# Optimization experiments

Hardware: AMD Instinct MI355X
Metric: run time of the kernel (lower is better)

The kernel has to match this reference:

```python
import jax, jax.numpy as jnp
import numpy as np

T, H, W_, CIN, LAT, HID, OUT, NHL = 32, 64, 64, 3, 256, 256, 3, 3
OMEGA = 30.0  # SIREN sine frequency


def _uniform(key, shape, fan_in):
    b = np.sqrt(6.0 / fan_in) / OMEGA
    return jax.random.uniform(key, shape, jnp.float32, -b, b)


def setup_inputs() -> dict:
    key = jax.random.key(0)
    ks = jax.random.split(key, 10)
    return {
        "coords": jax.random.normal(ks[0], (T, H, W_, CIN), jnp.float32),
        "latents": jax.random.normal(ks[1], (T, LAT), jnp.float32),
        # shared SIREN weights (nf_net): W stored as (out, in) like nn.Linear
        "W0": _uniform(ks[2], (HID, CIN), CIN),
        "b0": jnp.zeros((HID,), jnp.float32),
        "Wh": _uniform(ks[3], (NHL, HID, HID), HID),
        "bh": jnp.zeros((NHL, HID), jnp.float32),
        "Wf": _uniform(ks[4], (OUT, HID), HID),
        "bf": jnp.zeros((OUT,), jnp.float32),
        # hypernet weight generators (hw_net), no bias
        "HW0": _uniform(ks[5], (HID * CIN, LAT), LAT),
        "HWh": _uniform(ks[6], (NHL, HID * HID, LAT), LAT),
        # hypernet bias generators (hb_net), no bias
        "HB": _uniform(ks[7], (NHL + 1, HID, LAT), LAT),
    }


def reference(coords, latents, W0, b0, Wh, bh, Wf, bf, HW0, HWh, HB):
    t = latents.shape[0]
    # per-frame hyper biases for all layers: (t, NHL+1, HID)
    hb = jnp.einsum('tl,khl->tkh', latents, HB)
    # layer 0: per-frame weight (t, HID, CIN)
    hw0 = (latents @ HW0.T).reshape(t, HID, CIN)
    x = coords  # (t,h,w,CIN)
    x = (x @ W0.T + b0
         + jnp.einsum('thwi,toi->thwo', x, hw0)
         + hb[:, 0][:, None, None, :])
    x = jnp.sin(OMEGA * x)
    for i in range(NHL):
        hw = (latents @ HWh[i].T).reshape(t, HID, HID)  # (t, HID, HID)
        x = (x @ Wh[i].T + bh[i]
             + jnp.einsum('thwi,toi->thwo', x, hw)
             + hb[:, i + 1][:, None, None, :])
        x = jnp.sin(OMEGA * x)
    return x @ Wf.T + bf  # (t,h,w,OUT)
```

## Files before the change

### kernel.cpp

```cpp
#include <hip/hip_runtime.h>
#include <cstdint>
#include <cstddef>

typedef __attribute__((ext_vector_type(8))) _Float16 f16x8;
typedef __attribute__((ext_vector_type(16))) float f32x16;

#define LO_SCALE 2048.0f
#define LO_INV   (1.0f / 2048.0f)

union H8 { f16x8 v; _Float16 h[8]; };

__global__ __launch_bounds__(256) void kc_small(
    const float* __restrict__ latents, const float* __restrict__ W0,
    const float* __restrict__ b0, const float* __restrict__ bh,
    const float* __restrict__ HW0, const float* __restrict__ HB,
    _Float16* __restrict__ w0blob, float* __restrict__ beff) {
  int id = blockIdx.x * 256 + threadIdx.x;
  if (id < 32768) {
    int t = id >> 10, rem = id & 1023;
    int r2 = rem & 127, part = r2 >> 6, lane = r2 & 63;
    int nf = rem >> 7;
    int o = nf * 32 + (lane & 31), kc = lane >> 5;
    const float* lat = latents + t * 256;
    H8 outv;
#pragma unroll
    for (int j = 0; j < 8; ++j) outv.h[j] = (_Float16)0.0f;
#pragma unroll
    for (int j = 0; j < 8; ++j) {
      int i = kc * 8 + j;
      if (i < 3) {
        const float* row = HW0 + (o * 3 + i) * 256;
        float s = W0[o * 3 + i];
        for (int k = 0; k < 256; k += 4)
          s += row[k] * lat[k] + row[k + 1] * lat[k + 1] +
               row[k + 2] * lat[k + 2] + row[k + 3] * lat[k + 3];
        _Float16 hi = (_Float16)s;
        outv.h[j] = part ? (_Float16)((s - (float)hi) * LO_SCALE) : hi;
      }
    }
    *(f16x8*)(w0blob + (size_t)id * 8) = outv.v;
  } else {
    int v = id - 32768;
    int t = v >> 10, k = (v >> 8) & 3, hm = v & 255;
    float base = (k == 0) ? b0[hm] : bh[(k - 1) * 256 + hm];
    const float* lat = latents + t * 256;
    const float* row = HB + (size_t)(k * 256 + hm) * 256;
    float s = base;
    for (int kk = 0; kk < 256; kk += 4)
      s += row[kk] * lat[kk] + row[kk + 1] * lat[kk + 1] +
           row[kk + 2] * lat[kk + 2] + row[kk + 3] * lat[kk + 3];
    beff[v] = s;
  }
}

__global__ __launch_bounds__(256) void ka_weff_blob(
    const float* __restrict__ latents, const float* __restrict__ Wh,
    const float* __restrict__ HWh, _Float16* __restrict__ whblob) {
  __shared__ float lat_t[8192];
  int tid = threadIdx.x, bid = blockIdx.x;
  int h = bid & 1, ks = (bid >> 1) & 15, nf = (bid >> 5) & 7, l = bid >> 8;

  {
    int f = tid >> 3, kb = (tid & 7) * 32;
#pragma unroll
    for (int m = 0; m < 32; m += 4) {
      float4 v = *(const float4*)(latents + f * 256 + kb + m);
      lat_t[(kb + m + 0) * 32 + f] = v.x;
      lat_t[(kb + m + 1) * 32 + f] = v.y;
      lat_t[(kb + m + 2) * 32 + f] = v.z;
      lat_t[(kb + m + 3) * 32 + f] = v.w;
    }
  }
  __syncthreads();

  int oo = tid >> 3, jj = tid & 7;
  int o = nf * 32 + oo;
  int i = ks * 16 + h * 8 + jj;
  int r = o * 256 + i;
  const float* rowp = HWh + ((size_t)l * 65536 + (size_t)r) * 256;

  float acc[32];
#pragma unroll
  for (int f = 0; f < 32; ++f) acc[f] = 0.f;

  float curf[16], nxtf[16];
#pragma unroll
  for (int q = 0; q < 4; ++q)
    *(float4*)(curf + q * 4) = *(const float4*)(rowp + q * 4);

  for (int kc = 0; kc < 16; ++kc) {
    if (kc < 15) {
#pragma unroll
      for (int q = 0; q < 4; ++q)
        *(float4*)(nxtf + q * 4) = *(const float4*)(rowp + (kc + 1) * 16 + q * 4);
    }
    const float* lp = lat_t + kc * 512;
#pragma unroll
    for (int m = 0; m < 16; ++m) {
      float hw = curf[m];
#pragma unroll
      for (int fq = 0; fq < 8; ++fq) {
        float4 lv = *(const float4*)(lp + m * 32 + fq * 4);
        acc[fq * 4 + 0] += hw * lv.x;
        acc[fq * 4 + 1] += hw * lv.y;
        acc[fq * 4 + 2] += hw * lv.z;
        acc[fq * 4 + 3] += hw * lv.w;
      }
    }
#pragma unroll
    for (int q = 0; q < 16; ++q) curf[q] = nxtf[q];
  }

  float whv = Wh[l * 65536 + r];
  size_t cbase = (size_t)(nf * 16 + ks) * 1024 + (size_t)h * 256 + (size_t)tid;
#pragma unroll
  for (int t = 0; t < 32; ++t) {
    float w = acc[t] + whv;
    _Float16 hi = (_Float16)w;
    _Float16 lo = (_Float16)((w - (float)hi) * LO_SCALE);
    size_t b = (size_t)(t * 3 + l) * 131072 + cbase;
    whblob[b] = hi;
    whblob[b + 512] = lo;
  }
}

__global__ __launch_bounds__(512, 4) void kb_siren(
    const float* __restrict__ coords, const _Float16* __restrict__ whblob,
    const _Float16* __restrict__ w0blob, const float* __restrict__ beff,
    const float* __restrict__ Wf, const float* __restrict__ bf,
    float* __restrict__ out) {
  __shared__ _Float16 xs_hi[64 * 264];
  __shared__ _Float16 xs_lo[64 * 264];
  __shared__ float wf_s[768];
  __shared__ float red[1536];
  int tid = threadIdx.x;
  int bid0 = blockIdx.x;
  int bid = (bid0 & 7) * 256 + (bid0 >> 3);
  int t = bid >> 6, tile = bid & 63;
  int wv = tid >> 6, lane = tid & 63, col = lane & 31, h = lane >> 5;

  if (tid < 192) *(float4*)(wf_s + tid * 4) = *(const float4*)(Wf + tid * 4);
  if (tid < 64) {
    const float* cp = coords + (size_t)(t * 4096 + tile * 64 + tid) * 3;
    float c0 = cp[0], c1 = cp[1], c2 = cp[2];
    H8 hv, lv, z;
#pragma unroll
    for (int j = 0; j < 8; ++j) { hv.h[j] = (_Float16)0.f; lv.h[j] = (_Float16)0.f; z.h[j] = (_Float16)0.f; }
    _Float16 h0 = (_Float16)c0, h1 = (_Float16)c1, h2 = (_Float16)c2;
    hv.h[0] = h0; hv.h[1] = h1; hv.h[2] = h2;
    lv.h[0] = (_Float16)((c0 - (float)h0) * LO_SCALE);
    lv.h[1] = (_Float16)((c1 - (float)h1) * LO_SCALE);
    lv.h[2] = (_Float16)((c2 - (float)h2) * LO_SCALE);
    *(f16x8*)(xs_hi + tid * 264) = hv.v;
    *(f16x8*)(xs_lo + tid * 264) = lv.v;
    *(f16x8*)(xs_hi + tid * 264 + 8) = z.v;
    *(f16x8*)(xs_lo + tid * 264 + 8) = z.v;
  }
  __syncthreads();

  f32x16 accA[2], accB[2];

  auto init_bias = [&](int bk) {
    const float* bp = beff + ((t * 4 + bk) << 8) + wv * 32 + h * 4;
#pragma unroll
    for (int rq = 0; rq < 4; ++rq) {
      float4 bvv = *(const float4*)(bp + rq * 8);
      float ba[4];
      *(float4*)ba = bvv;
#pragma unroll
      for (int q = 0; q < 4; ++q) {
        accA[0][rq * 4 + q] = ba[q];
        accA[1][rq * 4 + q] = ba[q];
        accB[0][rq * 4 + q] = 0.f;
        accB[1][rq * 4 + q] = 0.f;
      }
    }
  };

  auto load_a = [&](const _Float16* blobL, int NS, int ks, f16x8 (&a)[2]) {
    const _Float16* p = blobL + (size_t)((wv * NS + ks) * 2) * 512 + lane * 8;
    a[0] = *(const f16x8*)p;
    a[1] = *(const f16x8*)(p + 512);
  };

  auto load_b = [&](int ks, f16x8 (&b)[2][2]) {
#pragma unroll
    for (int pf = 0; pf < 2; ++pf) {
      int off = (pf * 32 + col) * 264 + ks * 16 + h * 8;
      b[pf][0] = *(const f16x8*)(xs_hi + off);
      b[pf][1] = *(const f16x8*)(xs_lo + off);
    }
  };

  auto mfma6 = [&](f16x8 (&a)[2], f16x8 (&b)[2][2]) {
    accA[0] = __builtin_amdgcn_mfma_f32_32x32x16_f16(a[0], b[0][0], accA[0], 0, 0, 0);
    accA[1] = __builtin_amdgcn_mfma_f32_32x32x16_f16(a[0], b[1][0], accA[1], 0, 0, 0);
    accB[0] = __builtin_amdgcn_mfma_f32_32x32x16_f16(a[0], b[0][1], accB[0], 0, 0, 0);
    accB[1] = __builtin_amdgcn_mfma_f32_32x32x16_f16(a[0], b[1][1], accB[1], 0, 0, 0);
    accB[0] = __builtin_amdgcn_mfma_f32_32x32x16_f16(a[1], b[0][0], accB[0], 0, 0, 0);
    accB[1] = __builtin_amdgcn_mfma_f32_32x32x16_f16(a[1], b[1][0], accB[1], 0, 0, 0);
  };

  auto epilogue = [&]() {
#pragma unroll
    for (int pf = 0; pf < 2; ++pf)
#pragma unroll
      for (int r = 0; r < 16; ++r)
        accA[pf][r] = __sinf(30.0f * (accA[pf][r] + accB[pf][r] * LO_INV));
    __syncthreads();
#pragma unroll
    for (int pf = 0; pf < 2; ++pf)
#pragma unroll
      for (int g = 0; g < 2; ++g) {
        float seq[8];
#pragma unroll
        for (int q = 0; q < 4; ++q) {
          float oa = accA[pf][8 * g + q];
          float ob = accA[pf][8 * g + 4 + q];
          float send = h ? oa : ob;
          float recv = __shfl_xor(send, 32, 64);
          seq[q]     = h ? recv : oa;
          seq[4 + q] = h ? ob : recv;
        }
        H8 hv, lv;
#pragma unroll
        for (int j = 0; j < 8; ++j) {
          _Float16 hi = (_Float16)seq[j];
          hv.h[j] = hi;
          lv.h[j] = (_Float16)((seq[j] - (float)hi) * LO_SCALE);
        }
        int off = (pf * 32 + col) * 264 + wv * 32 + g * 16 + h * 8;
        *(f16x8*)(xs_hi + off) = hv.v;
        *(f16x8*)(xs_lo + off) = lv.v;
      }
    __syncthreads();
  };

  init_bias(0);
  {
    f16x8 a[2], b[2][2];
    load_a(w0blob + (size_t)t * 8192, 1, 0, a);
    load_b(0, b);
    mfma6(a, b);
  }
  epilogue();

  for (int li = 0; li < 3; ++li) {
    init_bias(li + 1);
    const _Float16* bl = whblob + (size_t)(t * 3 + li) * 131072;
#pragma unroll
    for (int ks = 0; ks < 16; ++ks) {
      f16x8 a[2], b[2][2];
      load_a(bl, 16, ks, a);
      load_b(ks, b);
      mfma6(a, b);
    }
    epilogue();
  }

  {
    float pc0 = 0.f, pc1 = 0.f, pc2 = 0.f;
    int px = tid & 63, kq = tid >> 6;
#pragma unroll
    for (int cc = 0; cc < 4; ++cc) {
      int k0 = kq * 32 + cc * 8;
      H8 hv, lv;
      hv.v = *(const f16x8*)(xs_hi + px * 264 + k0);
      lv.v = *(const f16x8*)(xs_lo + px * 264 + k0);
#pragma unroll
      for (int j = 0; j < 8; ++j) {
        float xv = (float)hv.h[j] + (float)lv.h[j] * LO_INV;
        pc0 += xv * wf_s[k0 + j];
        pc1 += xv * wf_s[256 + k0 + j];
        pc2 += xv * wf_s[512 + k0 + j];
      }
    }
    red[(kq * 64 + px) * 3 + 0] = pc0;
    red[(kq * 64 + px) * 3 + 1] = pc1;
    red[(kq * 64 + px) * 3 + 2] = pc2;
    __syncthreads();
    if (tid < 192) {
      int p2 = tid / 3, c = tid - p2 * 3;
      float s = bf[c];
#pragma unroll
      for (int q = 0; q < 8; ++q) s += red[(q * 64 + p2) * 3 + c];
      out[(size_t)(t * 4096 + tile * 64 + p2) * 3 + c] = s;
    }
  }
}

extern "C" void kernel_launch(void* const* d_in, const int* in_sizes, int n_in,
                              void* d_out, int out_size, void* d_ws, size_t ws_size,
                              hipStream_t stream) {
  const float* coords  = (const float*)d_in[0];
  const float* latents = (const float*)d_in[1];
  const float* W0      = (const float*)d_in[2];
  const float* b0      = (const float*)d_in[3];
  const float* Wh      = (const float*)d_in[4];
  const float* bh      = (const float*)d_in[5];
  const float* Wf      = (const float*)d_in[6];
  const float* bf      = (const float*)d_in[7];
  const float* HW0     = (const float*)d_in[8];
  const float* HWh     = (const float*)d_in[9];
  const float* HB      = (const float*)d_in[10];
  float* outp = (float*)d_out;

  char* w = (char*)d_ws;
  _Float16* whblob = (_Float16*)w;
  _Float16* w0blob = (_Float16*)(w + 25165824);
  float*    beff   = (float*)(w + 25690112);

  kc_small<<<256, 256, 0, stream>>>(latents, W0, b0, bh, HW0, HB, w0blob, beff);
  ka_weff_blob<<<768, 256, 0, stream>>>(latents, Wh, HWh, whblob);
  kb_siren<<<2048, 512, 0, stream>>>(coords, whblob, w0blob, beff, Wf, bf, outp);
}
```

Measured before the change: 242.1 us.

## Fuse prep kernels and halve SIREN pixel tile to raise occupancy

Merges the two hypernetwork weight-generation kernels into one launch by dispatching on block index, removing one launch and the serialization between them. The SIREN kernel now processes 32 pixels per block instead of 64, halving LDS and accumulator registers, doubling the grid, and raising the launch-bounds occupancy target. The final output projection reduction uses a cross-half shuffle before the LDS reduction. The trade-off is that each per-frame weight fragment is reused across half as many pixels, doubling weight traffic from cache/memory.

```diff
diff --git a/kernel.cpp b/kernel.cpp
--- a/kernel.cpp
+++ b/kernel.cpp
@@ -10,54 +10,56 @@
 
 union H8 { f16x8 v; _Float16 h[8]; };
 
-__global__ __launch_bounds__(256) void kc_small(
+__global__ __launch_bounds__(256) void kab(
     const float* __restrict__ latents, const float* __restrict__ W0,
     const float* __restrict__ b0, const float* __restrict__ bh,
     const float* __restrict__ HW0, const float* __restrict__ HB,
-    _Float16* __restrict__ w0blob, float* __restrict__ beff) {
-  int id = blockIdx.x * 256 + threadIdx.x;
-  if (id < 32768) {
-    int t = id >> 10, rem = id & 1023;
-    int r2 = rem & 127, part = r2 >> 6, lane = r2 & 63;
-    int nf = rem >> 7;
-    int o = nf * 32 + (lane & 31), kc = lane >> 5;
-    const float* lat = latents + t * 256;
-    H8 outv;
-#pragma unroll
-    for (int j = 0; j < 8; ++j) outv.h[j] = (_Float16)0.0f;
-#pragma unroll
-    for (int j = 0; j < 8; ++j) {
-      int i = kc * 8 + j;
-      if (i < 3) {
-        const float* row = HW0 + (o * 3 + i) * 256;
-        float s = W0[o * 3 + i];
-        for (int k = 0; k < 256; k += 4)
-          s += row[k] * lat[k] + row[k + 1] * lat[k + 1] +
-               row[k + 2] * lat[k + 2] + row[k + 3] * lat[k + 3];
-        _Float16 hi = (_Float16)s;
-        outv.h[j] = part ? (_Float16)((s - (float)hi) * LO_SCALE) : hi;
-      }
-    }
-    *(f16x8*)(w0blob + (size_t)id * 8) = outv.v;
-  } else {
-    int v = id - 32768;
-    int t = v >> 10, k = (v >> 8) & 3, hm = v & 255;
-    float base = (k == 0) ? b0[hm] : bh[(k - 1) * 256 + hm];
-    const float* lat = latents + t * 256;
-    const float* row = HB + (size_t)(k * 256 + hm) * 256;
-    float s = base;
-    for (int kk = 0; kk < 256; kk += 4)
-      s += row[kk] * lat[kk] + row[kk + 1] * lat[kk + 1] +
-           row[kk + 2] * lat[kk + 2] + row[kk + 3] * lat[kk + 3];
-    beff[v] = s;
-  }
-}
-
-__global__ __launch_bounds__(256) void ka_weff_blob(
-    const float* __restrict__ latents, const float* __restrict__ Wh,
-    const float* __restrict__ HWh, _Float16* __restrict__ whblob) {
+    const float* __restrict__ Wh, const float* __restrict__ HWh,
+    _Float16* __restrict__ w0blob, float* __restrict__ beff,
+    _Float16* __restrict__ whblob) {
   __shared__ float lat_t[8192];
   int tid = threadIdx.x, bid = blockIdx.x;
+
+  if (bid >= 768) {
+    int id = (bid - 768) * 256 + tid;
+    if (id < 32768) {
+      int t = id >> 10, rem = id & 1023;
+      int r2 = rem & 127, part = r2 >> 6, lane = r2 & 63;
+      int nf = rem >> 7;
+      int o = nf * 32 + (lane & 31), kc = lane >> 5;
+      const float* lat = latents + t * 256;
+      H8 outv;
+#pragma unroll
+      for (int j = 0; j < 8; ++j) outv.h[j] = (_Float16)0.0f;
+#pragma unroll
+      for (int j = 0; j < 8; ++j) {
+        int i = kc * 8 + j;
+        if (i < 3) {
+          const float* row = HW0 + (o * 3 + i) * 256;
+          float s = W0[o * 3 + i];
+          for (int k = 0; k < 256; k += 4)
+            s += row[k] * lat[k] + row[k + 1] * lat[k + 1] +
+                 row[k + 2] * lat[k + 2] + row[k + 3] * lat[k + 3];
+          _Float16 hi = (_Float16)s;
+          outv.h[j] = part ? (_Float16)((s - (float)hi) * LO_SCALE) : hi;
+        }
+      }
+      *(f16x8*)(w0blob + (size_t)id * 8) = outv.v;
+    } else {
+      int v = id - 32768;
+      int t = v >> 10, k = (v >> 8) & 3, hm = v & 255;
+      float base = (k == 0) ? b0[hm] : bh[(k - 1) * 256 + hm];
+      const float* lat = latents + t * 256;
+      const float* row = HB + (size_t)(k * 256 + hm) * 256;
+      float s = base;
+      for (int kk = 0; kk < 256; kk += 4)
+        s += row[kk] * lat[kk] + row[kk + 1] * lat[kk + 1] +
+             row[kk + 2] * lat[kk + 2] + row[kk + 3] * lat[kk + 3];
+      beff[v] = s;
+    }
+    return;
+  }
+
   int h = bid & 1, ks = (bid >> 1) & 15, nf = (bid >> 5) & 7, l = bid >> 8;
 
   {
@@ -124,24 +126,24 @@
   }
 }
 
-__global__ __launch_bounds__(512, 4) void kb_siren(
+__global__ __launch_bounds__(512, 6) void kb_siren(
     const float* __restrict__ coords, const _Float16* __restrict__ whblob,
     const _Float16* __restrict__ w0blob, const float* __restrict__ beff,
     const float* __restrict__ Wf, const float* __restrict__ bf,
     float* __restrict__ out) {
-  __shared__ _Float16 xs_hi[64 * 264];
-  __shared__ _Float16 xs_lo[64 * 264];
+  __shared__ _Float16 xs_hi[32 * 264];
+  __shared__ _Float16 xs_lo[32 * 264];
   __shared__ float wf_s[768];
-  __shared__ float red[1536];
+  __shared__ float red[768];
   int tid = threadIdx.x;
   int bid0 = blockIdx.x;
-  int bid = (bid0 & 7) * 256 + (bid0 >> 3);
-  int t = bid >> 6, tile = bid & 63;
+  int bid = (bid0 & 7) * 512 + (bid0 >> 3);
+  int t = bid >> 7, tile = bid & 127;
   int wv = tid >> 6, lane = tid & 63, col = lane & 31, h = lane >> 5;
 
   if (tid < 192) *(float4*)(wf_s + tid * 4) = *(const float4*)(Wf + tid * 4);
-  if (tid < 64) {
-    const float* cp = coords + (size_t)(t * 4096 + tile * 64 + tid) * 3;
+  if (tid < 32) {
+    const float* cp = coords + (size_t)(t * 4096 + tile * 32 + tid) * 3;
     float c0 = cp[0], c1 = cp[1], c2 = cp[2];
     H8 hv, lv, z;
 #pragma unroll
@@ -158,7 +160,7 @@
   }
   __syncthreads();
 
-  f32x16 accA[2], accB[2];
+  f32x16 accA, accB;
 
   auto init_bias = [&](int bk) {
     const float* bp = beff + ((t * 4 + bk) << 8) + wv * 32 + h * 4;
@@ -169,10 +171,8 @@
       *(float4*)ba = bvv;
 #pragma unroll
       for (int q = 0; q < 4; ++q) {
-        accA[0][rq * 4 + q] = ba[q];
-        accA[1][rq * 4 + q] = ba[q];
-        accB[0][rq * 4 + q] = 0.f;
-        accB[1][rq * 4 + q] = 0.f;
+        accA[rq * 4 + q] = ba[q];
+        accB[rq * 4 + q] = 0.f;
       }
     }
   };
@@ -183,65 +183,55 @@
     a[1] = *(const f16x8*)(p + 512);
   };
 
-  auto load_b = [&](int ks, f16x8 (&b)[2][2]) {
-#pragma unroll
-    for (int pf = 0; pf < 2; ++pf) {
-      int off = (pf * 32 + col) * 264 + ks * 16 + h * 8;
-      b[pf][0] = *(const f16x8*)(xs_hi + off);
-      b[pf][1] = *(const f16x8*)(xs_lo + off);
-    }
-  };
-
-  auto mfma6 = [&](f16x8 (&a)[2], f16x8 (&b)[2][2]) {
-    accA[0] = __builtin_amdgcn_mfma_f32_32x32x16_f16(a[0], b[0][0], accA[0], 0, 0, 0);
-    accA[1] = __builtin_amdgcn_mfma_f32_32x32x16_f16(a[0], b[1][0], accA[1], 0, 0, 0);
-    accB[0] = __builtin_amdgcn_mfma_f32_32x32x16_f16(a[0], b[0][1], accB[0], 0, 0, 0);
-    accB[1] = __builtin_amdgcn_mfma_f32_32x32x16_f16(a[0], b[1][1], accB[1], 0, 0, 0);
-    accB[0] = __builtin_amdgcn_mfma_f32_32x32x16_f16(a[1], b[0][0], accB[0], 0, 0, 0);
-    accB[1] = __builtin_amdgcn_mfma_f32_32x32x16_f16(a[1], b[1][0], accB[1], 0, 0, 0);
+  auto load_b = [&](int ks, f16x8 (&b)[2]) {
+    int off = col * 264 + ks * 16 + h * 8;
+    b[0] = *(const f16x8*)(xs_hi + off);
+    b[1] = *(const f16x8*)(xs_lo + off);
+  };
+
+  auto mfma3 = [&](f16x8 (&a)[2], f16x8 (&b)[2]) {
+    accA = __builtin_amdgcn_mfma_f32_32x32x16_f16(a[0], b[0], accA, 0, 0, 0);
+    accB = __builtin_amdgcn_mfma_f32_32x32x16_f16(a[0], b[1], accB, 0, 0, 0);
+    accB = __builtin_amdgcn_mfma_f32_32x32x16_f16(a[1], b[0], accB, 0, 0, 0);
   };
 
   auto epilogue = [&]() {
 #pragma unroll
-    for (int pf = 0; pf < 2; ++pf)
-#pragma unroll
-      for (int r = 0; r < 16; ++r)
-        accA[pf][r] = __sinf(30.0f * (accA[pf][r] + accB[pf][r] * LO_INV));
+    for (int r = 0; r < 16; ++r)
+      accA[r] = __sinf(30.0f * (accA[r] + accB[r] * LO_INV));
     __syncthreads();
 #pragma unroll
-    for (int pf = 0; pf < 2; ++pf)
-#pragma unroll
-      for (int g = 0; g < 2; ++g) {
-        float seq[8];
-#pragma unroll
-        for (int q = 0; q < 4; ++q) {
-          float oa = accA[pf][8 * g + q];
-          float ob = accA[pf][8 * g + 4 + q];
-          float send = h ? oa : ob;
-          float recv = __shfl_xor(send, 32, 64);
-          seq[q]     = h ? recv : oa;
-          seq[4 + q] = h ? ob : recv;
-        }
-        H8 hv, lv;
-#pragma unroll
-        for (int j = 0; j < 8; ++j) {
-          _Float16 hi = (_Float16)seq[j];
-          hv.h[j] = hi;
-          lv.h[j] = (_Float16)((seq[j] - (float)hi) * LO_SCALE);
-        }
-        int off = (pf * 32 + col) * 264 + wv * 32 + g * 16 + h * 8;
-        *(f16x8*)(xs_hi + off) = hv.v;
-        *(f16x8*)(xs_lo + off) = lv.v;
-      }
+    for (int g = 0; g < 2; ++g) {
+      float seq[8];
+#pragma unroll
+      for (int q = 0; q < 4; ++q) {
+        float oa = accA[8 * g + q];
+        float ob = accA[8 * g + 4 + q];
+        float send = h ? oa : ob;
+        float recv = __shfl_xor(send, 32, 64);
+        seq[q]     = h ? recv : oa;
+        seq[4 + q] = h ? ob : recv;
+      }
+      H8 hv, lv;
+#pragma unroll
+      for (int j = 0; j < 8; ++j) {
+        _Float16 hi = (_Float16)seq[j];
+        hv.h[j] = hi;
+        lv.h[j] = (_Float16)((seq[j] - (float)hi) * LO_SCALE);
+      }
+      int off = col * 264 + wv * 32 + g * 16 + h * 8;
+      *(f16x8*)(xs_hi + off) = hv.v;
+      *(f16x8*)(xs_lo + off) = lv.v;
+    }
     __syncthreads();
   };
 
   init_bias(0);
   {
-    f16x8 a[2], b[2][2];
+    f16x8 a[2], b[2];
     load_a(w0blob + (size_t)t * 8192, 1, 0, a);
     load_b(0, b);
-    mfma6(a, b);
+    mfma3(a, b);
   }
   epilogue();
 
@@ -250,20 +240,20 @@
     const _Float16* bl = whblob + (size_t)(t * 3 + li) * 131072;
 #pragma unroll
     for (int ks = 0; ks < 16; ++ks) {
-      f16x8 a[2], b[2][2];
+      f16x8 a[2], b[2];
       load_a(bl, 16, ks, a);
       load_b(ks, b);
-      mfma6(a, b);
+      mfma3(a, b);
     }
     epilogue();
   }
 
   {
     float pc0 = 0.f, pc1 = 0.f, pc2 = 0.f;
-    int px = tid & 63, kq = tid >> 6;
-#pragma unroll
-    for (int cc = 0; cc < 4; ++cc) {
-      int k0 = kq * 32 + cc * 8;
+    int px = tid & 31, kq = tid >> 5;
+#pragma unroll
+    for (int cc = 0; cc < 2; ++cc) {
+      int k0 = kq * 16 + cc * 8;
       H8 hv, lv;
       hv.v = *(const f16x8*)(xs_hi + px * 264 + k0);
       lv.v = *(const f16x8*)(xs_lo + px * 264 + k0);
@@ -275,16 +265,21 @@
         pc2 += xv * wf_s[512 + k0 + j];
       }
     }
-    red[(kq * 64 + px) * 3 + 0] = pc0;
-    red[(kq * 64 + px) * 3 + 1] = pc1;
-    red[(kq * 64 + px) * 3 + 2] = pc2;
+    pc0 += __shfl_xor(pc0, 32, 64);
+    pc1 += __shfl_xor(pc1, 32, 64);
+    pc2 += __shfl_xor(pc2, 32, 64);
+    if (h == 0) {
+      red[wv * 96 + px * 3 + 0] = pc0;
+      red[wv * 96 + px * 3 + 1] = pc1;
+      red[wv * 96 + px * 3 + 2] = pc2;
+    }
     __syncthreads();
-    if (tid < 192) {
+    if (tid < 96) {
       int p2 = tid / 3, c = tid - p2 * 3;
       float s = bf[c];
 #pragma unroll
-      for (int q = 0; q < 8; ++q) s += red[(q * 64 + p2) * 3 + c];
-      out[(size_t)(t * 4096 + tile * 64 + p2) * 3 + c] = s;
+      for (int q = 0; q < 8; ++q) s += red[q * 96 + p2 * 3 + c];
+      out[(size_t)(t * 4096 + tile * 32 + p2) * 3 + c] = s;
     }
   }
 }
@@ -310,7 +305,7 @@
   _Float16* w0blob = (_Float16*)(w + 25165824);
   float*    beff   = (float*)(w + 25690112);
 
-  kc_small<<<256, 256, 0, stream>>>(latents, W0, b0, bh, HW0, HB, w0blob, beff);
-  ka_weff_blob<<<768, 256, 0, stream>>>(latents, Wh, HWh, whblob);
-  kb_siren<<<2048, 512, 0, stream>>>(coords, whblob, w0blob, beff, Wf, bf, outp);
+  kab<<<1024, 256, 0, stream>>>(latents, W0, b0, bh, HW0, HB, Wh, HWh,
+                                w0blob, beff, whblob);
+  kb_siren<<<4096, 512, 0, stream>>>(coords, whblob, w0blob, beff, Wf, bf, outp);
 }
```

Measured after the change: 258.7 us. 1.07x slower.
